# Optimization experiments

Hardware: AMD Instinct MI355X
Metric: run time of the kernel (lower is better)

Reference implementation:

```python
import jax, jax.numpy as jnp
import numpy as np

H = 16        # num heads
DH = 64       # dim per head
M = 256       # num landmarks
ITERS = 6     # Moore-Penrose iterations
K = 13        # residual depthwise conv kernel size


def setup_inputs() -> dict:
    key = jax.random.key(0)
    k1, k2, k3, k4 = jax.random.split(key, 4)
    b, n, dim = 4, 4096, 1024
    inner = H * DH
    x = jax.random.normal(k1, (b, n, dim), dtype=jnp.float32)
    w_qkv = jax.random.normal(k2, (dim, 3 * inner), dtype=jnp.float32) * 0.02
    w_conv = jax.random.normal(k3, (H, 1, K, 1), dtype=jnp.float32) * 0.1
    w_fc = jax.random.normal(k4, (inner, dim), dtype=jnp.float32) * 0.02
    b_fc = jnp.zeros((dim,), dtype=jnp.float32)
    return {"x": x, "w_qkv": w_qkv, "w_conv": w_conv, "w_fc": w_fc, "b_fc": b_fc}


def moore_penrose_inverse(a, iters=ITERS):
    # a: [b, h, m, m]
    a_abs = jnp.abs(a)
    col = a_abs.sum(axis=-1)
    row = a_abs.sum(axis=-2)
    z = jnp.swapaxes(a, -1, -2) / (jnp.max(col) * jnp.max(row))
    I = jnp.eye(a.shape[-1], dtype=a.dtype)
    for _ in range(iters):
        az = a @ z
        z = 0.25 * z @ (13 * I - az @ (15 * I - az @ (7 * I - az)))
    return z


def reference(x, w_qkv, w_conv, w_fc, b_fc):
    b, n, dim = x.shape
    scale = DH ** -0.5
    qkv = x @ w_qkv                                   # [b, n, 3*inner]
    q, k, v = jnp.split(qkv, 3, axis=-1)
    split_heads = lambda t: t.reshape(b, n, H, DH).transpose(0, 2, 1, 3)  # [b,h,n,d]
    q, k, v = split_heads(q) * scale, split_heads(k), split_heads(v)

    # landmarks: mean over groups of l = n/m consecutive tokens (no mask)
    l = n // M
    q_l = q.reshape(b, H, M, l, DH).sum(axis=3) / l   # [b,h,m,d]
    k_l = k.reshape(b, H, M, l, DH).sum(axis=3) / l

    sim1 = jnp.einsum('bhid,bhjd->bhij', q, k_l)      # [b,h,n,m]
    sim2 = jnp.einsum('bhid,bhjd->bhij', q_l, k_l)    # [b,h,m,m]
    sim3 = jnp.einsum('bhid,bhjd->bhij', q_l, k)      # [b,h,m,n]

    attn1 = jax.nn.softmax(sim1, axis=-1)
    attn2 = jax.nn.softmax(sim2, axis=-1)
    attn3 = jax.nn.softmax(sim3, axis=-1)

    attn2_inv = moore_penrose_inverse(attn2)
    out = (attn1 @ attn2_inv) @ (attn3 @ v)           # [b,h,n,d]

    # depthwise residual conv over sequence dim, kernel (K,1), groups=h
    res = jax.lax.conv_general_dilated(
        out, w_conv, window_strides=(1, 1),
        padding=((K // 2, K // 2), (0, 0)),
        feature_group_count=H,
        dimension_numbers=('NCHW', 'OIHW', 'NCHW'))
    out = out + res

    out = out.transpose(0, 2, 1, 3).reshape(b, n, H * DH)
    out = out @ w_fc + b_fc                           # [b, n, dim]
    return out
```

## Files before the change

kernel.cpp:

```cpp
#include <hip/hip_runtime.h>


typedef _Float16 h16;
typedef __attribute__((ext_vector_type(4))) float    f32x4;
typedef __attribute__((ext_vector_type(8))) _Float16 h16x8;
typedef __attribute__((ext_vector_type(4))) _Float16 h16x4;

struct GArgs {
  const h16* A; int lda; long abatch;
  const h16* B; int ldb; long bbatch;
  int M, N, K;
  float alpha, beta;
  const h16* auxh; long auxhb;
  float* of32; long ofb;
  h16* oh;  long ohb;
  h16* oht; long ohtb;
  const float* bias;
  h16* q; h16* k; h16* vt;
};

template<int BM,int BN,int WM,int WN,bool QKV>
__launch_bounds__((BM/WM)*(BN/WN)*64)
__global__ void gemm_k(GArgs g)
{
  constexpr int NWN = BN/WN;
  constexpr int FM = WM/16, FN = WN/16;
  constexpr int TH = (BM/WM)*NWN*64;
  constexpr int LA = (BM*32)/(TH*8);
  constexpr int LB = (BN*32)/(TH*8);
  __shared__ __align__(16) h16 As[BM][40];
  __shared__ __align__(16) h16 Bs[BN][40];
  const int tid = threadIdx.x;
  const int wv = tid >> 6, lane = tid & 63;
  const int wm = wv / NWN, wn = wv % NWN;
  const int l16 = lane & 15, lk = lane >> 4;
  const long bm = (long)blockIdx.y * BM;
  const long bn = (long)blockIdx.x * BN;
  const int bat = blockIdx.z;
  const h16* Ab = g.A + (long)bat * g.abatch;
  const h16* Bb = g.B + (long)bat * g.bbatch;

  f32x4 acc[FM][FN] = {};

  for (int k0 = 0; k0 < g.K; k0 += 32) {
    __syncthreads();
    #pragma unroll
    for (int i = 0; i < LA; ++i) {
      const int e = (i*TH + tid) * 8;
      const int r = e >> 5, c = e & 31;
      *(f32x4*)(&As[r][c]) = *(const f32x4*)(Ab + (bm + r)*(long)g.lda + k0 + c);
    }
    #pragma unroll
    for (int i = 0; i < LB; ++i) {
      const int e = (i*TH + tid) * 8;
      const int r = e >> 5, c = e & 31;
      *(f32x4*)(&Bs[r][c]) = *(const f32x4*)(Bb + (bn + r)*(long)g.ldb + k0 + c);
    }
    __syncthreads();
    h16x8 af[FM], bf[FN];
    #pragma unroll
    for (int m = 0; m < FM; ++m)
      af[m] = *(const h16x8*)(&As[wm*WM + m*16 + l16][lk*8]);
    #pragma unroll
    for (int n = 0; n < FN; ++n)
      bf[n] = *(const h16x8*)(&Bs[wn*WN + n*16 + l16][lk*8]);
    #pragma unroll
    for (int m = 0; m < FM; ++m)
      #pragma unroll
      for (int n = 0; n < FN; ++n)
        acc[m][n] = __builtin_amdgcn_mfma_f32_16x16x32_f16(af[m], bf[n], acc[m][n], 0, 0, 0);
  }

  const long r0 = bm + wm*WM;
  const long c0 = bn + wn*WN;
  #pragma unroll
  for (int m = 0; m < FM; ++m) {
    #pragma unroll
    for (int n = 0; n < FN; ++n) {
      #pragma unroll
      for (int rr = 0; rr < 4; ++rr) {
        const long row = r0 + m*16 + lk*4 + rr;
        const long col = c0 + n*16 + l16;
        float v = acc[m][n][rr];
        if (QKV) {
          const int b   = (int)(row >> 12);
          const int nn  = (int)(row & 4095);
          const int whc = (int)(col >> 10);
          const int rem = (int)(col & 1023);
          const int hh = rem >> 6, dd = rem & 63;
          const long bh = (long)b*16 + hh;
          if (whc == 0)      g.q [(bh*4096 + nn)*64 + dd] = (h16)(v * 0.125f);
          else if (whc == 1) g.k [(bh*4096 + nn)*64 + dd] = (h16)v;
          else               g.vt[(bh*64 + dd)*4096 + nn] = (h16)v;
        } else {
          v *= g.alpha;
          if (g.auxh) v += g.beta * (float)g.auxh[(long)bat*g.auxhb + row*(long)g.N + col];
          if (g.bias) v += g.bias[col];
          if (g.of32) g.of32[(long)bat*g.ofb  + row*(long)g.N + col] = v;
          if (g.oh)   g.oh  [(long)bat*g.ohb  + row*(long)g.N + col] = (h16)v;
          if (g.oht)  g.oht [(long)bat*g.ohtb + col*(long)g.M + row] = (h16)v;
        }
      }
    }
  }
}

__launch_bounds__(256)
__global__ void sm256_k(const float* __restrict__ inp, h16* __restrict__ oh,
                        float* __restrict__ o32)
{
  const int wid = threadIdx.x >> 6, lane = threadIdx.x & 63;
  const long row = (long)blockIdx.x*4 + wid;
  float v[4];
  *(f32x4*)v = *(const f32x4*)(inp + row*256 + lane*4);
  float mx = fmaxf(fmaxf(v[0],v[1]), fmaxf(v[2],v[3]));
  for (int o = 32; o; o >>= 1) mx = fmaxf(mx, __shfl_xor(mx, o, 64));
  float sm = 0.f;
  #pragma unroll
  for (int j = 0; j < 4; ++j) { v[j] = __expf(v[j]-mx); sm += v[j]; }
  for (int o = 32; o; o >>= 1) sm += __shfl_xor(sm, o, 64);
  const float inv = 1.0f/sm;
  h16x4 t; f32x4 t2;
  #pragma unroll
  for (int u = 0; u < 4; ++u) { t[u] = (h16)(v[u]*inv); t2[u] = v[u]*inv; }
  *(h16x4*)(oh + row*256 + lane*4) = t;
  *(f32x4*)(o32 + row*256 + lane*4) = t2;
}

__global__ void landmark_k(const h16* __restrict__ in, h16* __restrict__ out)
{
  const long i = (long)blockIdx.x*256 + threadIdx.x;
  const int d = (int)(i & 63);
  const long m = (i >> 6) & 255;
  const long bh = i >> 14;
  const h16* p = in + (bh*4096 + m*16)*64 + d;
  float s = 0.f;
  #pragma unroll
  for (int j = 0; j < 16; ++j) s += (float)p[j*64];
  out[i] = (h16)(s * 0.0625f);
}

__global__ void a_scale_k(const float* __restrict__ a, float* scal)
{
  const int bh = blockIdx.x, t = threadIdx.x;
  const float* p = a + (long)bh*65536;
  float cs = 0.f, rs = 0.f;
  for (int i = 0; i < 256; ++i) cs += p[(long)i*256 + t];
  for (int j = 0; j < 256; ++j) rs += p[(long)t*256 + j];
  for (int o = 32; o; o >>= 1) { cs = fmaxf(cs, __shfl_xor(cs,o,64)); rs = fmaxf(rs, __shfl_xor(rs,o,64)); }
  __shared__ float red[8];
  if ((t & 63) == 0) { red[t>>6] = cs; red[4+(t>>6)] = rs; }
  __syncthreads();
  if (t == 0) {
    float c = fmaxf(fmaxf(red[0],red[1]),fmaxf(red[2],red[3]));
    float r = fmaxf(fmaxf(red[4],red[5]),fmaxf(red[6],red[7]));
    atomicMax((int*)scal,     __float_as_int(c));
    atomicMax((int*)(scal+1), __float_as_int(r));
  }
}

__global__ void init_k(float* s) { if (threadIdx.x < 2) s[threadIdx.x] = 0.f; }

__global__ void z0_k(const float* __restrict__ a, const float* __restrict__ scal,
                     h16* __restrict__ zh, h16* __restrict__ zt)
{
  __shared__ float t[64][65];
  const int bh = blockIdx.y;
  const int i0 = (blockIdx.x >> 2)*64, j0 = (blockIdx.x & 3)*64;
  const float inv = 1.0f/(scal[0]*scal[1]);
  const long base = (long)bh*65536;
  const int tt = threadIdx.x;
  for (int it = 0; it < 16; ++it) {
    const int e = it*256 + tt;
    const int r = e >> 6, c = e & 63;
    const float v = a[base + (long)(j0+r)*256 + i0 + c];
    t[r][c] = v;
    zt[base + (long)(j0+r)*256 + i0 + c] = (h16)(v*inv);
  }
  __syncthreads();
  for (int it = 0; it < 16; ++it) {
    const int e = it*256 + tt;
    const int r = e >> 6, c = e & 63;
    zh[base + (long)(i0+r)*256 + j0 + c] = (h16)(t[c][r]*inv);
  }
}

__launch_bounds__(256)
__global__ void flash_av_k(const h16* __restrict__ ql, const h16* __restrict__ kh,
                           const h16* __restrict__ vt, h16* __restrict__ avt)
{
  __shared__ __align__(16) h16 Ks[64][72];
  __shared__ __align__(16) h16 Vs[64][72];
  __shared__ __align__(16) h16 Ps[4][16][72];
  const int tid = threadIdx.x;
  const int wv = tid>>6, lane = tid&63, l16 = lane&15, lk = lane>>4;
  const int bx = blockIdx.x;
  const int bh   = (bx&7)*8 + ((bx>>3)&7);
  const int mblk = bx>>6;
  const int row0 = mblk*64 + wv*16;
  h16x8 af[2];
  {
    const h16* qp = ql + (long)bh*16384 + (long)(row0 + l16)*64;
    af[0] = *(const h16x8*)(qp + lk*8);
    af[1] = *(const h16x8*)(qp + 32 + lk*8);
  }
  const int sr = tid>>3, sc = (tid&7)*8;
  const h16* kbase = kh + (long)bh*262144;
  const h16* vbase = vt + (long)bh*262144;
  float m_st[4], l_st[4];
  f32x4 acc[4] = {};
  #pragma unroll
  for (int r = 0; r < 4; ++r) { m_st[r] = -1e30f; l_st[r] = 0.f; }

  for (int jt = 0; jt < 64; ++jt) {
    __syncthreads();
    *(f32x4*)(&Ks[sr][sc])    = *(const f32x4*)(kbase + (long)(jt*64+sr)*64 + sc);
    *(f32x4*)(&Ks[sr+32][sc]) = *(const f32x4*)(kbase + (long)(jt*64+sr+32)*64 + sc);
    *(f32x4*)(&Vs[sr][sc])    = *(const f32x4*)(vbase + (long)sr*4096 + jt*64 + sc);
    *(f32x4*)(&Vs[sr+32][sc]) = *(const f32x4*)(vbase + (long)(sr+32)*4096 + jt*64 + sc);
    __syncthreads();
    f32x4 sacc[4];
    #pragma unroll
    for (int n = 0; n < 4; ++n) {
      h16x8 b0 = *(const h16x8*)(&Ks[n*16+l16][lk*8]);
      h16x8 b1 = *(const h16x8*)(&Ks[n*16+l16][32+lk*8]);
      f32x4 s = {};
      s = __builtin_amdgcn_mfma_f32_16x16x32_f16(af[0], b0, s, 0,0,0);
      s = __builtin_amdgcn_mfma_f32_16x16x32_f16(af[1], b1, s, 0,0,0);
      sacc[n] = s;
    }
    float pexp[4][4];
    #pragma unroll
    for (int rr = 0; rr < 4; ++rr) {
      float tm = fmaxf(fmaxf(sacc[0][rr],sacc[1][rr]), fmaxf(sacc[2][rr],sacc[3][rr]));
      #pragma unroll
      for (int o = 1; o < 16; o <<= 1) tm = fmaxf(tm, __shfl_xor(tm, o, 64));
      const float mn = fmaxf(m_st[rr], tm);
      const float scl = __expf(m_st[rr] - mn);
      m_st[rr] = mn;
      float ts = 0.f;
      #pragma unroll
      for (int n = 0; n < 4; ++n) { float e = __expf(sacc[n][rr]-mn); pexp[n][rr] = e; ts += e; }
      #pragma unroll
      for (int o = 1; o < 16; o <<= 1) ts += __shfl_xor(ts, o, 64);
      l_st[rr] = l_st[rr]*scl + ts;
      #pragma unroll
      for (int n = 0; n < 4; ++n) acc[n][rr] *= scl;
    }
    #pragma unroll
    for (int n = 0; n < 4; ++n)
      #pragma unroll
      for (int rr = 0; rr < 4; ++rr)
        Ps[wv][lk*4+rr][n*16+l16] = (h16)pexp[n][rr];
    #pragma unroll
    for (int kk = 0; kk < 2; ++kk) {
      h16x8 pa = *(const h16x8*)(&Ps[wv][l16][kk*32+lk*8]);
      #pragma unroll
      for (int n = 0; n < 4; ++n) {
        h16x8 vf = *(const h16x8*)(&Vs[n*16+l16][kk*32+lk*8]);
        acc[n] = __builtin_amdgcn_mfma_f32_16x16x32_f16(pa, vf, acc[n], 0,0,0);
      }
    }
  }
  #pragma unroll
  for (int n = 0; n < 4; ++n)
    #pragma unroll
    for (int rr = 0; rr < 4; ++rr) {
      const int d = n*16+l16, rw = row0 + lk*4 + rr;
      avt[(long)bh*16384 + (long)d*256 + rw] = (h16)(acc[n][rr] / l_st[rr]);
    }
}

__launch_bounds__(256)
__global__ void flash_out_k(const h16* __restrict__ qh, const h16* __restrict__ kl,
                            const h16* __restrict__ zavt, float* __restrict__ outp)
{
  __shared__ __align__(16) h16 Ps[4][16][264];
  const int tid = threadIdx.x;
  const int wv = tid>>6, lane = tid&63, l16 = lane&15, lk = lane>>4;
  const int bh = blockIdx.y;
  const int row0 = blockIdx.x*64 + wv*16;
  h16x8 af[2];
  {
    const h16* qp = qh + (long)bh*262144 + (long)(row0+l16)*64;
    af[0] = *(const h16x8*)(qp + lk*8);
    af[1] = *(const h16x8*)(qp + 32 + lk*8);
  }
  const h16* kp = kl + (long)bh*16384;
  f32x4 sacc[16];
  #pragma unroll
  for (int n = 0; n < 16; ++n) {
    h16x8 b0 = *(const h16x8*)(kp + (long)(n*16+l16)*64 + lk*8);
    h16x8 b1 = *(const h16x8*)(kp + (long)(n*16+l16)*64 + 32 + lk*8);
    f32x4 s = {};
    s = __builtin_amdgcn_mfma_f32_16x16x32_f16(af[0], b0, s, 0,0,0);
    s = __builtin_amdgcn_mfma_f32_16x16x32_f16(af[1], b1, s, 0,0,0);
    sacc[n] = s;
  }
  float l_st[4];
  #pragma unroll
  for (int rr = 0; rr < 4; ++rr) {
    float tm = sacc[0][rr];
    #pragma unroll
    for (int n = 1; n < 16; ++n) tm = fmaxf(tm, sacc[n][rr]);
    #pragma unroll
    for (int o = 1; o < 16; o <<= 1) tm = fmaxf(tm, __shfl_xor(tm, o, 64));
    float ts = 0.f;
    #pragma unroll
    for (int n = 0; n < 16; ++n) {
      float e = __expf(sacc[n][rr]-tm);
      ts += e;
      Ps[wv][lk*4+rr][n*16+l16] = (h16)e;
    }
    #pragma unroll
    for (int o = 1; o < 16; o <<= 1) ts += __shfl_xor(ts, o, 64);
    l_st[rr] = ts;
  }
  const h16* zp = zavt + (long)bh*16384;
  f32x4 acc[4] = {};
  #pragma unroll
  for (int kk = 0; kk < 8; ++kk) {
    h16x8 pa = *(const h16x8*)(&Ps[wv][l16][kk*32+lk*8]);
    #pragma unroll
    for (int n = 0; n < 4; ++n) {
      h16x8 vf = *(const h16x8*)(zp + (long)(n*16+l16)*256 + kk*32 + lk*8);
      acc[n] = __builtin_amdgcn_mfma_f32_16x16x32_f16(pa, vf, acc[n], 0,0,0);
    }
  }
  #pragma unroll
  for (int n = 0; n < 4; ++n)
    #pragma unroll
    for (int rr = 0; rr < 4; ++rr)
      outp[(long)bh*262144 + (long)(row0+lk*4+rr)*64 + n*16+l16] = acc[n][rr]/l_st[rr];
}

__global__ void conv_res_k(const float* __restrict__ o, const float* __restrict__ wc,
                           h16* __restrict__ y)
{
  const long i = (long)blockIdx.x*256 + threadIdx.x;
  const int d  = (int)(i & 63);
  const int nn = (int)((i >> 6) & 4095);
  const long bh = i >> 18;
  const int h = (int)(bh & 15);
  const long b = bh >> 4;
  const float* base = o + bh*262144 + d;
  float acc = base[(long)nn*64];
  #pragma unroll
  for (int t = 0; t < 13; ++t) {
    const int n2 = nn + t - 6;
    if (0 <= n2 && n2 < 4096) acc += wc[h*13 + t] * base[(long)n2*64];
  }
  y[((b*4096 + nn)*16 + h)*64 + d] = (h16)acc;
}

__global__ void cvt_k(const float* __restrict__ x, h16* __restrict__ o)
{
  const long i = ((long)blockIdx.x*256 + threadIdx.x)*4;
  f32x4 v = *(const f32x4*)(x + i);
  h16x4 t;
  #pragma unroll
  for (int u = 0; u < 4; ++u) t[u] = (h16)v[u];
  *(h16x4*)(o + i) = t;
}

__global__ void tcvt_k(const float* __restrict__ in, h16* __restrict__ out, int R, int C)
{
  __shared__ h16 t[64][74];
  const int r0 = blockIdx.y*64, c0 = blockIdx.x*64;
  const int tt = threadIdx.x;
  for (int it = 0; it < 16; ++it) {
    const int e = it*256 + tt;
    const int r = e >> 6, c = e & 63;
    t[r][c] = (h16)in[(long)(r0+r)*C + c0 + c];
  }
  __syncthreads();
  for (int it = 0; it < 16; ++it) {
    const int e = it*256 + tt;
    const int r = e >> 6, c = e & 63;
    out[(long)(c0+r)*R + r0 + c] = t[c][r];
  }
}

static inline void g_gen(hipStream_t st, bool wide, int batches,
  const h16* A, int lda, long ab, const h16* B, int ldb, long bb,
  int M, int N, int K, float alpha, float beta, const h16* auxh, long auxhb,
  float* of32, long ofb, h16* oh, long ohb, h16* oht, long ohtb, const float* bias)
{
  GArgs g{A,lda,ab,B,ldb,bb,M,N,K,alpha,beta,auxh,auxhb,of32,ofb,oh,ohb,oht,ohtb,bias,
          nullptr,nullptr,nullptr};
  if (wide) { dim3 gr(N/128, M/128, batches); gemm_k<128,128,64,64,false><<<gr,256,0,st>>>(g); }
  else      { dim3 gr(N/64,  M/128, batches); gemm_k<128,64, 32,64,false><<<gr,256,0,st>>>(g); }
}

extern "C" void kernel_launch(void* const* d_in, const int* in_sizes, int n_in,
                              void* d_out, int out_size, void* d_ws, size_t ws_size,
                              hipStream_t stream)
{
  const float* x      = (const float*)d_in[0];
  const float* w_qkv  = (const float*)d_in[1];
  const float* w_conv = (const float*)d_in[2];
  const float* w_fc   = (const float*)d_in[3];
  const float* b_fc   = (const float*)d_in[4];
  float* out = (float*)d_out;
  char* ws = (char*)d_ws;

  h16*   xh    = (h16*)(ws + 0L);
  h16*   wqkvT = (h16*)(ws + 33554432L);
  h16*   wfcT  = (h16*)(ws + 39845888L);
  h16*   qh    = (h16*)(ws + 41943040L);
  h16*   kh    = (h16*)(ws + 75497472L);
  h16*   vt    = (h16*)(ws + 109051904L);
  h16*   ql    = (h16*)(ws + 142606336L);
  h16*   kl    = (h16*)(ws + 144703488L);
  float* af32  = (float*)(ws + 146800640L);
  h16*   ah    = (h16*)(ws + 163577856L);
  h16*   zh0   = (h16*)(ws + 171966464L);
  h16*   zt0   = (h16*)(ws + 180355072L);
  h16*   zh1   = (h16*)(ws + 188743680L);
  h16*   zt1   = (h16*)(ws + 197132288L);
  h16*   azh   = (h16*)(ws + 205520896L);
  h16*   azt   = (h16*)(ws + 213909504L);
  h16*   w1t   = (h16*)(ws + 222298112L);
  h16*   w2t   = (h16*)(ws + 230686720L);
  h16*   avt   = (h16*)(ws + 239075328L);
  h16*   zavt  = (h16*)(ws + 241172480L);
  float* scal  = (float*)(ws + 243269632L);
  h16*   zh[2] = {zh0, zh1};
  h16*   zt[2] = {zt0, zt1};
  h16*   yh    = xh;
  float* attn_out = out;

  cvt_k<<<16384, 256, 0, stream>>>(x, xh);
  { dim3 gr(48, 16); tcvt_k<<<gr, 256, 0, stream>>>(w_qkv, wqkvT, 1024, 3072); }
  { dim3 gr(16, 16); tcvt_k<<<gr, 256, 0, stream>>>(w_fc, wfcT, 1024, 1024); }
  init_k<<<1, 64, 0, stream>>>(scal);

  {
    GArgs g{xh,1024,0, wqkvT,1024,0, 16384,3072,1024, 1.f,0.f,
            nullptr,0, nullptr,0, nullptr,0, nullptr,0, nullptr, qh, kh, vt};
    dim3 gr(24, 128, 1);
    gemm_k<128,128,64,64,true><<<gr, 256, 0, stream>>>(g);
  }

  landmark_k<<<4096, 256, 0, stream>>>(qh, ql);
  landmark_k<<<4096, 256, 0, stream>>>(kh, kl);

  g_gen(stream, true, 64, ql,64,16384, kl,64,16384, 256,256,64,
        1.f,0.f, nullptr,0, af32,65536, nullptr,0, nullptr,0, nullptr);
  sm256_k<<<4096, 256, 0, stream>>>(af32, ah, af32);

  a_scale_k<<<64, 256, 0, stream>>>(af32, scal);
  { dim3 gr(16, 64); z0_k<<<gr, 256, 0, stream>>>(af32, scal, zh[0], zt[0]); }

  int cur = 0;
  for (int it = 0; it < 6; ++it) {
    g_gen(stream, true, 64, ah,256,65536, zt[cur],256,65536, 256,256,256,
          1.f,0.f, nullptr,0, nullptr,0, azh,65536, azt,65536, nullptr);
    g_gen(stream, true, 64, azh,256,65536, azt,256,65536, 256,256,256,
          -1.f,7.f, azh,65536, nullptr,0, nullptr,0, w1t,65536, nullptr);
    g_gen(stream, true, 64, azh,256,65536, w1t,256,65536, 256,256,256,
          -1.f,15.f, azh,65536, nullptr,0, nullptr,0, w2t,65536, nullptr);
    const int nxt = cur ^ 1;
    g_gen(stream, true, 64, zh[cur],256,65536, w2t,256,65536, 256,256,256,
          -0.25f,3.25f, zh[cur],65536, nullptr,0, zh[nxt],65536, zt[nxt],65536, nullptr);
    cur = nxt;
  }

  flash_av_k<<<256, 256, 0, stream>>>(ql, kh, vt, avt);

  g_gen(stream, false, 64, zh[cur],256,65536, avt,256,16384, 256,64,256,
        1.f,0.f, nullptr,0, nullptr,0, nullptr,0, zavt,16384, nullptr);

  { dim3 gr(64, 64); flash_out_k<<<gr, 256, 0, stream>>>(qh, kl, zavt, attn_out); }

  conv_res_k<<<65536, 256, 0, stream>>>(attn_out, w_conv, yh);

  g_gen(stream, true, 1, yh,1024,0, wfcT,1024,0, 16384,1024,1024,
        1.f,0.f, nullptr,0, out,0, nullptr,0, nullptr,0, b_fc);

  (void)in_sizes; (void)n_in; (void)out_size; (void)ws_size;
}
```

Before: 1.457 ms.

## Fuse Moore-Penrose iteration GEMMs into one persistent per-head kernel

Replaces the 24 separate batched GEMM launches of the six Moore-Penrose iterations with a single kernel. It uses one 512-thread block per batch-head, and each block runs all 24 256x256x256 GEMMs sequentially through shared-memory tiles. Intermediates still go through global memory, separated by block barriers. The aim is to remove per-launch overhead and inter-kernel gaps. The cost is that only 64 blocks run, leaving most CUs idle, and the transposed output stores are uncoalesced.

New measurement: 2.136 ms. +46.6%, slower.

```diff
diff --git a/kernel.cpp b/kernel.cpp
--- a/kernel.cpp
+++ b/kernel.cpp
@@ -105,6 +105,88 @@
   }
 }
 
+typedef h16 (*lds_t)[72];
+
+__device__ __forceinline__ void blk_gemm(
+    lds_t As, lds_t Bs,
+    const h16* __restrict__ Ag, const h16* __restrict__ Bg,
+    const h16* __restrict__ auxg, float aa, float ab,
+    h16* __restrict__ oN, h16* __restrict__ oT, int tid)
+{
+  const int wv = tid >> 6, lane = tid & 63;
+  const int wm = wv >> 2, wn = wv & 3;
+  const int l16 = lane & 15, lk = lane >> 4;
+  f32x4 acc[8][4] = {};
+  for (int k0 = 0; k0 < 256; k0 += 64) {
+    __syncthreads();
+    #pragma unroll
+    for (int i = 0; i < 4; ++i) {
+      const int e = (i*512 + tid) * 8;
+      const int r = e >> 6, c = e & 63;
+      *(f32x4*)(&As[r][c]) = *(const f32x4*)(Ag + r*256 + k0 + c);
+      *(f32x4*)(&Bs[r][c]) = *(const f32x4*)(Bg + r*256 + k0 + c);
+    }
+    __syncthreads();
+    #pragma unroll
+    for (int kk = 0; kk < 2; ++kk) {
+      h16x8 af[8], bf[4];
+      #pragma unroll
+      for (int m = 0; m < 8; ++m)
+        af[m] = *(const h16x8*)(&As[wm*128 + m*16 + l16][kk*32 + lk*8]);
+      #pragma unroll
+      for (int n = 0; n < 4; ++n)
+        bf[n] = *(const h16x8*)(&Bs[wn*64 + n*16 + l16][kk*32 + lk*8]);
+      #pragma unroll
+      for (int m = 0; m < 8; ++m)
+        #pragma unroll
+        for (int n = 0; n < 4; ++n)
+          acc[m][n] = __builtin_amdgcn_mfma_f32_16x16x32_f16(af[m], bf[n], acc[m][n], 0,0,0);
+    }
+  }
+  #pragma unroll
+  for (int m = 0; m < 8; ++m)
+    #pragma unroll
+    for (int n = 0; n < 4; ++n)
+      #pragma unroll
+      for (int rr = 0; rr < 4; ++rr) {
+        const int row = wm*128 + m*16 + lk*4 + rr;
+        const int col = wn*64 + n*16 + l16;
+        float v = aa * acc[m][n][rr];
+        if (auxg) v += ab * (float)auxg[row*256 + col];
+        if (oN) oN[row*256 + col] = (h16)v;
+        if (oT) oT[col*256 + row] = (h16)v;
+      }
+  __syncthreads();
+}
+
+__launch_bounds__(512)
+__global__ void mp_fused_k(const h16* __restrict__ a_,
+                           h16* __restrict__ yh_, h16* __restrict__ yt_,
+                           h16* __restrict__ w1_, h16* __restrict__ w2_,
+                           h16* __restrict__ zh0_, h16* __restrict__ zt0_,
+                           h16* __restrict__ zh1_, h16* __restrict__ zt1_)
+{
+  __shared__ __align__(16) h16 As[256][72];
+  __shared__ __align__(16) h16 Bs[256][72];
+  const int tid = threadIdx.x;
+  const long off = (long)blockIdx.x * 65536;
+  const h16* A = a_ + off;
+  h16* Y  = yh_ + off;  h16* Yt = yt_ + off;
+  h16* W1 = w1_ + off;  h16* W2 = w2_ + off;
+  h16* z0h = zh0_ + off; h16* z0t = zt0_ + off;
+  h16* z1h = zh1_ + off; h16* z1t = zt1_ + off;
+  for (int it = 0; it < 3; ++it) {
+    blk_gemm(As,Bs, A,   z0t, nullptr, 1.f,   0.f,   Y,    Yt,  tid);
+    blk_gemm(As,Bs, Y,   Yt,  Y,      -1.f,   7.f,   nullptr, W1, tid);
+    blk_gemm(As,Bs, Y,   W1,  Y,      -1.f,  15.f,   nullptr, W2, tid);
+    blk_gemm(As,Bs, z0h, W2,  z0h,    -0.25f, 3.25f, z1h, z1t, tid);
+    blk_gemm(As,Bs, A,   z1t, nullptr, 1.f,   0.f,   Y,    Yt,  tid);
+    blk_gemm(As,Bs, Y,   Yt,  Y,      -1.f,   7.f,   nullptr, W1, tid);
+    blk_gemm(As,Bs, Y,   W1,  Y,      -1.f,  15.f,   nullptr, W2, tid);
+    blk_gemm(As,Bs, z1h, W2,  z1h,    -0.25f, 3.25f, z0h, z0t, tid);
+  }
+}
+
 __launch_bounds__(256)
 __global__ void sm256_k(const float* __restrict__ inp, h16* __restrict__ oh,
                         float* __restrict__ o32)
@@ -425,8 +507,6 @@
   h16*   avt   = (h16*)(ws + 239075328L);
   h16*   zavt  = (h16*)(ws + 241172480L);
   float* scal  = (float*)(ws + 243269632L);
-  h16*   zh[2] = {zh0, zh1};
-  h16*   zt[2] = {zt0, zt1};
   h16*   yh    = xh;
   float* attn_out = out;
 
@@ -450,25 +530,13 @@
   sm256_k<<<4096, 256, 0, stream>>>(af32, ah, af32);
 
   a_scale_k<<<64, 256, 0, stream>>>(af32, scal);
-  { dim3 gr(16, 64); z0_k<<<gr, 256, 0, stream>>>(af32, scal, zh[0], zt[0]); }
-
-  int cur = 0;
-  for (int it = 0; it < 6; ++it) {
-    g_gen(stream, true, 64, ah,256,65536, zt[cur],256,65536, 256,256,256,
-          1.f,0.f, nullptr,0, nullptr,0, azh,65536, azt,65536, nullptr);
-    g_gen(stream, true, 64, azh,256,65536, azt,256,65536, 256,256,256,
-          -1.f,7.f, azh,65536, nullptr,0, nullptr,0, w1t,65536, nullptr);
-    g_gen(stream, true, 64, azh,256,65536, w1t,256,65536, 256,256,256,
-          -1.f,15.f, azh,65536, nullptr,0, nullptr,0, w2t,65536, nullptr);
-    const int nxt = cur ^ 1;
-    g_gen(stream, true, 64, zh[cur],256,65536, w2t,256,65536, 256,256,256,
-          -0.25f,3.25f, zh[cur],65536, nullptr,0, zh[nxt],65536, zt[nxt],65536, nullptr);
-    cur = nxt;
-  }
+  { dim3 gr(16, 64); z0_k<<<gr, 256, 0, stream>>>(af32, scal, zh0, zt0); }
+
+  mp_fused_k<<<64, 512, 0, stream>>>(ah, azh, azt, w1t, w2t, zh0, zt0, zh1, zt1);
 
   flash_av_k<<<256, 256, 0, stream>>>(ql, kh, vt, avt);
 
-  g_gen(stream, false, 64, zh[cur],256,65536, avt,256,16384, 256,64,256,
+  g_gen(stream, false, 64, zh0,256,65536, avt,256,16384, 256,64,256,
         1.f,0.f, nullptr,0, nullptr,0, nullptr,0, zavt,16384, nullptr);
 
   { dim3 gr(64, 64); flash_out_k<<<gr, 256, 0, stream>>>(qh, kl, zavt, attn_out); }
```
